# Performance work log

Hardware: AMD Instinct MI355X
Metric: run time of the kernel (lower is better)

The kernel has to match this reference:

```python
import jax, jax.numpy as jnp
import numpy as np

MASK_NEG = 1e30


def setup_inputs() -> dict:
    key = jax.random.key(0)
    k_q, k_k, k_m, k_w1, k_w2, k_v = jax.random.split(key, 6)
    B, S, D, A = 32, 2048, 1024, 1024  # batch, seq, feature dim, attn dim
    # Xavier-uniform-like scale for weights
    lim = float(np.sqrt(6.0 / (D + A)))
    query = jax.random.normal(k_q, (B, D), dtype=jnp.float32)
    keys = jax.random.normal(k_k, (B, S, D), dtype=jnp.float32)
    mask = jax.random.randint(k_m, (B, S), 0, 2) > 0  # True = keep
    W1 = jax.random.uniform(k_w1, (A, D), jnp.float32, -lim, lim)
    W2 = jax.random.uniform(k_w2, (A, D), jnp.float32, -lim, lim)
    v = jax.random.uniform(k_v, (A,), jnp.float32, -lim, lim)
    return {"query": query, "keys": keys, "mask": mask, "W1": W1, "W2": W2, "v": v}


def reference(query, keys, mask, W1, W2, v):
    w1_query = jnp.einsum('bd,ad->ba', query, W1)          # (B, A)
    w2_keys = jnp.einsum('bsd,ad->bsa', keys, W2)          # (B, S, A)
    combined = jnp.tanh(w1_query[:, None, :] + w2_keys)    # (B, S, A)
    scores = jnp.einsum('bsa,a->bs', combined, v)          # (B, S)
    # masked softmax: subtract huge constant at masked-out positions
    scores = scores - (~mask).astype(scores.dtype) * MASK_NEG
    return jax.nn.softmax(scores, axis=-1)
```

## Files before the change

kernel.cpp:

```cpp
#include <hip/hip_runtime.h>
#include <hip/hip_bf16.h>
#include <stdint.h>

#define NB 32
#define NS 2048
#define ND 1024
#define NA 1024
#define MASK_NEG 1e30f

#define BM 256
#define BN 256
#define BK 64
#define NTILES 64

typedef __attribute__((ext_vector_type(4))) float f32x4;
typedef __attribute__((ext_vector_type(8))) __bf16 bf16x8;

__device__ __forceinline__ void glds16(const void* g, void* l) {
  __builtin_amdgcn_global_load_lds(
      (const __attribute__((address_space(1))) uint32_t*)g,
      (__attribute__((address_space(3))) uint32_t*)(uintptr_t)l, 16, 0, 0);
}

__global__ void zero_f32(float* __restrict__ p, int n) {
  int i = blockIdx.x * 256 + threadIdx.x;
  if (i < n) p[i] = 0.f;
}

__global__ __launch_bounds__(256) void cvt_bf16(const float* __restrict__ in,
                                                __bf16* __restrict__ out, int n8) {
  long i = blockIdx.x * 256 + threadIdx.x;
  const long stride = (long)gridDim.x * 256;
  for (; i < n8; i += stride) {
    f32x4 a = ((const f32x4*)in)[2 * i];
    f32x4 b = ((const f32x4*)in)[2 * i + 1];
    bf16x8 o;
#pragma unroll
    for (int j = 0; j < 4; ++j) { o[j] = (__bf16)a[j]; o[4 + j] = (__bf16)b[j]; }
    ((bf16x8*)out)[i] = o;
  }
}

__global__ __launch_bounds__(256) void w1q_kernel(const float* __restrict__ q,
                                                  const float* __restrict__ W1,
                                                  float* __restrict__ w1q) {
  const int b = blockIdx.x;
  const int a0 = blockIdx.y * 64;
  const int t = threadIdx.x;
  const int al = t >> 2;
  const int part = t & 3;
  const float* wrow = W1 + (size_t)(a0 + al) * ND + part * 256;
  const float* qrow = q + (size_t)b * ND + part * 256;
  float sum = 0.f;
#pragma unroll 8
  for (int i = 0; i < 256; i += 4) {
    float4 w = *reinterpret_cast<const float4*>(wrow + i);
    float4 x = *reinterpret_cast<const float4*>(qrow + i);
    sum += w.x * x.x + w.y * x.y + w.z * x.z + w.w * x.w;
  }
  __shared__ float red[256];
  red[t] = sum;
  __syncthreads();
  if (t < 64) {
    w1q[(size_t)b * NA + a0 + t] = red[t * 4] + red[t * 4 + 1] + red[t * 4 + 2] + red[t * 4 + 3];
  }
}

__global__ __launch_bounds__(512, 1) void score_gemm(
    const float* __restrict__ keysf, const __bf16* __restrict__ W2b,
    const float* __restrict__ w1q, const float* __restrict__ vvec,
    float* __restrict__ scores) {
  __shared__ __attribute__((aligned(1024))) char ldsA[6 * 16384];
  __shared__ __attribute__((aligned(1024))) char ldsB[4 * 16384];

  const int t = threadIdx.x;
  const int bs0 = blockIdx.x * BM;
  const int b = bs0 >> 11;
  const int lane = t & 63;
  const int wid = t >> 6;
  const int wr = wid >> 1;
  const int wc = wid & 1;
  const int lrow = lane & 15;
  const int ko = lane >> 4;

  const int rowA = t >> 4;
  const int scolA = (t & 15) ^ (rowA & 15);
  const int rowB = t >> 3;
  const int scolB = (t & 7) ^ (rowB & 7);

  const int sA00 = (ko * 2) ^ lrow, sA01 = (ko * 2 + 1) ^ lrow;
  const int sA10 = (8 + ko * 2) ^ lrow, sA11 = (8 + ko * 2 + 1) ^ lrow;
  const int sB0 = ko ^ (lrow & 7), sB1 = (4 + ko) ^ (lrow & 7);

  f32x4 acc[4][8];
#pragma unroll
  for (int mi = 0; mi < 4; ++mi)
#pragma unroll
    for (int ni = 0; ni < 8; ++ni) acc[mi][ni] = f32x4{0.f, 0.f, 0.f, 0.f};

  bf16x8 af[4][2], bfr[2][2];

#define STAGE_A(T, Q)                                                           \
  do {                                                                          \
    if ((T) < NTILES) {                                                         \
      const unsigned slot_ = (4u * (unsigned)(T) + (unsigned)(Q)) % 6u;         \
      char* d_ = ldsA + slot_ * 16384 + t * 16;                                 \
      const size_t r0_ = (size_t)(bs0 + (Q)*64 + rowA);                         \
      const int kf_ = ((T)&15) * 64 + scolA * 4;                                \
      glds16(keysf + r0_ * ND + kf_, d_);                                       \
      glds16(keysf + (r0_ + 32) * ND + kf_, d_ + 8192);                         \
    }                                                                           \
  } while (0)

#define STAGE_B(T, H)                                                           \
  do {                                                                          \
    if ((T) < NTILES) {                                                         \
      const unsigned slot_ = (2u * (unsigned)(T) + (unsigned)(H)) % 4u;         \
      char* d_ = ldsB + slot_ * 16384 + t * 16;                                 \
      const size_t r0_ = (size_t)(((T) >> 4) * 256 + (H)*128 + rowB);           \
      const int ke_ = (((T)&15) * 64) + scolB * 8;                              \
      glds16(W2b + r0_ * ND + ke_, d_);                                         \
      glds16(W2b + (r0_ + 64) * ND + ke_, d_ + 8192);                           \
    }                                                                           \
  } while (0)

#define SB_ __builtin_amdgcn_sched_barrier(0)
#define P1 __builtin_amdgcn_s_setprio(1)
#define P0 __builtin_amdgcn_s_setprio(0)
#define BAR __builtin_amdgcn_s_barrier()

#define PHASE(P_, STAGES)                                                       \
  do {                                                                          \
    STAGES;                                                                     \
    if ((P_) == 0) {                                                            \
      const char* Ab_ = ldsA + ((4u * (unsigned)tau + (unsigned)wr) % 6u) * 16384; \
      _Pragma("unroll") for (int mi = 0; mi < 4; ++mi) {                        \
        const int rb_ = (mi * 16 + lrow) * 256;                                 \
        f32x4 l0 = *reinterpret_cast<const f32x4*>(Ab_ + rb_ + sA00 * 16);      \
        f32x4 l1 = *reinterpret_cast<const f32x4*>(Ab_ + rb_ + sA01 * 16);      \
        f32x4 h0 = *reinterpret_cast<const f32x4*>(Ab_ + rb_ + sA10 * 16);      \
        f32x4 h1 = *reinterpret_cast<const f32x4*>(Ab_ + rb_ + sA11 * 16);      \
        _Pragma("unroll") for (int j = 0; j < 4; ++j) {                         \
          af[mi][0][j] = (__bf16)l0[j]; af[mi][0][4 + j] = (__bf16)l1[j];       \
          af[mi][1][j] = (__bf16)h0[j]; af[mi][1][4 + j] = (__bf16)h1[j];       \
        }                                                                       \
      }                                                                         \
    }                                                                           \
    {                                                                           \
      const char* Bb_ = ldsB + ((2u * (unsigned)tau + (unsigned)wc) % 4u) * 16384; \
      _Pragma("unroll") for (int nq = 0; nq < 2; ++nq) {                        \
        const int rb_ = (((P_)*2 + nq) * 16 + lrow) * 128;                      \
        bfr[nq][0] = *reinterpret_cast<const bf16x8*>(Bb_ + rb_ + sB0 * 16);    \
        bfr[nq][1] = *reinterpret_cast<const bf16x8*>(Bb_ + rb_ + sB1 * 16);    \
      }                                                                         \
    }                                                                           \
    BAR;                                                                        \
    asm volatile("s_waitcnt lgkmcnt(0)");                                       \
    SB_;                                                                        \
    P1;                                                                         \
    _Pragma("unroll") for (int mi = 0; mi < 4; ++mi)                            \
        _Pragma("unroll") for (int nq = 0; nq < 2; ++nq) {                      \
      acc[mi][(P_)*2 + nq] = __builtin_amdgcn_mfma_f32_16x16x32_bf16(           \
          af[mi][0], bfr[nq][0], acc[mi][(P_)*2 + nq], 0, 0, 0);                \
      acc[mi][(P_)*2 + nq] = __builtin_amdgcn_mfma_f32_16x16x32_bf16(           \
          af[mi][1], bfr[nq][1], acc[mi][(P_)*2 + nq], 0, 0, 0);                \
    }                                                                           \
    P0;                                                                         \
    if ((P_) == 3) {                                                            \
      asm volatile("s_waitcnt vmcnt(0)");                                       \
      SB_;                                                                      \
    }                                                                           \
    BAR;                                                                        \
  } while (0)

  STAGE_A(0, 0);
  STAGE_A(0, 1);
  STAGE_A(0, 2);
  STAGE_A(0, 3);
  STAGE_B(0, 0);
  STAGE_B(0, 1);
  __syncthreads();

  for (int tau = 0; tau < NTILES; ++tau) {
    PHASE(0, { STAGE_A(tau + 1, 0); STAGE_A(tau + 1, 1); STAGE_B(tau + 1, 0); });
    PHASE(1, { STAGE_A(tau + 1, 2); STAGE_A(tau + 1, 3); STAGE_B(tau + 1, 1); });
    PHASE(2, {});
    PHASE(3, {});

    if ((tau & 15) == 15) {
      const int a0 = (tau >> 4) * BN;
      float w1v[8], vv[8];
#pragma unroll
      for (int ni = 0; ni < 8; ++ni) {
        const int a = a0 + wc * 128 + ni * 16 + lrow;
        w1v[ni] = w1q[(size_t)b * NA + a];
        vv[ni] = vvec[a];
      }
#pragma unroll
      for (int mi = 0; mi < 4; ++mi)
#pragma unroll
        for (int r = 0; r < 4; ++r) {
          float p = 0.f;
#pragma unroll
          for (int ni = 0; ni < 8; ++ni) {
            const float x = acc[mi][ni][r] + w1v[ni];
            const float e = __expf(2.f * x);
            p += (1.f - 2.f * __builtin_amdgcn_rcpf(e + 1.f)) * vv[ni];
          }
          p += __shfl_xor(p, 1);
          p += __shfl_xor(p, 2);
          p += __shfl_xor(p, 4);
          p += __shfl_xor(p, 8);
          if (lrow == 0)
            atomicAdd(&scores[bs0 + wr * 64 + mi * 16 + ko * 4 + r], p);
        }
#pragma unroll
      for (int mi = 0; mi < 4; ++mi)
#pragma unroll
        for (int ni = 0; ni < 8; ++ni) acc[mi][ni] = f32x4{0.f, 0.f, 0.f, 0.f};
    }
  }

#undef STAGE_A
#undef STAGE_B
#undef PHASE
#undef SB_
#undef P1
#undef P0
#undef BAR
}

__global__ __launch_bounds__(256) void softmax_kernel(const float* __restrict__ scores,
                                                      const int* __restrict__ mask,
                                                      float* __restrict__ out) {
  const int b = blockIdx.x;
  const int t = threadIdx.x;
  float sc[8];
  float mx = -3.4e38f;
#pragma unroll
  for (int j = 0; j < 8; ++j) {
    int i = t + j * 256;
    float s = scores[b * NS + i];
    if (mask[b * NS + i] == 0) s -= MASK_NEG;
    sc[j] = s;
    mx = fmaxf(mx, s);
  }
#pragma unroll
  for (int off = 1; off < 64; off <<= 1) mx = fmaxf(mx, __shfl_xor(mx, off));
  __shared__ float redm[4];
  __shared__ float reds[4];
  if ((t & 63) == 0) redm[t >> 6] = mx;
  __syncthreads();
  mx = fmaxf(fmaxf(redm[0], redm[1]), fmaxf(redm[2], redm[3]));
  float e[8];
  float sum = 0.f;
#pragma unroll
  for (int j = 0; j < 8; ++j) {
    e[j] = __expf(sc[j] - mx);
    sum += e[j];
  }
#pragma unroll
  for (int off = 1; off < 64; off <<= 1) sum += __shfl_xor(sum, off);
  if ((t & 63) == 0) reds[t >> 6] = sum;
  __syncthreads();
  sum = reds[0] + reds[1] + reds[2] + reds[3];
  float inv = 1.f / sum;
#pragma unroll
  for (int j = 0; j < 8; ++j) out[b * NS + t + j * 256] = e[j] * inv;
}

extern "C" void kernel_launch(void* const* d_in, const int* in_sizes, int n_in,
                              void* d_out, int out_size, void* d_ws, size_t ws_size,
                              hipStream_t stream) {
  const float* q = (const float*)d_in[0];
  const float* keysf = (const float*)d_in[1];
  const int* mask = (const int*)d_in[2];
  const float* W1 = (const float*)d_in[3];
  const float* W2f = (const float*)d_in[4];
  const float* v = (const float*)d_in[5];
  float* out = (float*)d_out;

  float* scores = (float*)d_ws;
  float* w1q = scores + NB * NS;
  __bf16* W2b = (__bf16*)(w1q + NB * NA);

  zero_f32<<<NB * NS / 256, 256, 0, stream>>>(scores, NB * NS);
  cvt_bf16<<<512, 256, 0, stream>>>(W2f, W2b, NA * ND / 8);
  w1q_kernel<<<dim3(NB, NA / 64), 256, 0, stream>>>(q, W1, w1q);
  score_gemm<<<NB * NS / BM, 512, 0, stream>>>(keysf, W2b, w1q, v, scores);
  softmax_kernel<<<NB, 256, 0, stream>>>(scores, mask, out);
}
```

Before: 221.2 us.

## Switch score GEMM from 16x16x32 to 32x32x16 bf16 MFMA tiles

Replaces the 16x16x32 MFMA micro-tiling with 32x32x16 MFMA instructions, reorganising the accumulators into 2x4 f32x16 blocks and reworking the LDS fragment loads and swizzle indexing to match. Each phase now issues 8 larger MFMAs over one k-substep instead of 16 small ones. The epilogue reduction is adapted to the 32-lane row layout, with an extra shuffle and new row indexing for the atomic adds. The aim is to cut the number of B-fragment LDS reads per MFMA and to use the instruction's higher operand reuse, at the cost of different LDS bank access patterns and register pressure.

```diff
diff --git a/kernel.cpp b/kernel.cpp
--- a/kernel.cpp
+++ b/kernel.cpp
@@ -14,6 +14,7 @@
 #define NTILES 64
 
 typedef __attribute__((ext_vector_type(4))) float f32x4;
+typedef __attribute__((ext_vector_type(16))) float f32x16;
 typedef __attribute__((ext_vector_type(8))) __bf16 bf16x8;
 
 __device__ __forceinline__ void glds16(const void* g, void* l) {
@@ -80,25 +81,25 @@
   const int wid = t >> 6;
   const int wr = wid >> 1;
   const int wc = wid & 1;
-  const int lrow = lane & 15;
-  const int ko = lane >> 4;
+  const int r31 = lane & 31;
+  const int hi = lane >> 5;
+  const int lrA = r31 & 15;
+  const int lrB = r31 & 7;
 
   const int rowA = t >> 4;
   const int scolA = (t & 15) ^ (rowA & 15);
   const int rowB = t >> 3;
   const int scolB = (t & 7) ^ (rowB & 7);
 
-  const int sA00 = (ko * 2) ^ lrow, sA01 = (ko * 2 + 1) ^ lrow;
-  const int sA10 = (8 + ko * 2) ^ lrow, sA11 = (8 + ko * 2 + 1) ^ lrow;
-  const int sB0 = ko ^ (lrow & 7), sB1 = (4 + ko) ^ (lrow & 7);
-
-  f32x4 acc[4][8];
-#pragma unroll
-  for (int mi = 0; mi < 4; ++mi)
-#pragma unroll
-    for (int ni = 0; ni < 8; ++ni) acc[mi][ni] = f32x4{0.f, 0.f, 0.f, 0.f};
-
-  bf16x8 af[4][2], bfr[2][2];
+  f32x16 acc[2][4];
+#pragma unroll
+  for (int mi = 0; mi < 2; ++mi)
+#pragma unroll
+    for (int nt = 0; nt < 4; ++nt)
+#pragma unroll
+      for (int r = 0; r < 16; ++r) acc[mi][nt][r] = 0.f;
+
+  bf16x8 af[2][4], bfr[4];
 
 #define STAGE_A(T, Q)                                                           \
   do {                                                                          \
@@ -129,44 +130,42 @@
 #define P0 __builtin_amdgcn_s_setprio(0)
 #define BAR __builtin_amdgcn_s_barrier()
 
-#define PHASE(P_, STAGES)                                                       \
+#define PHASE(KS_, STAGES)                                                      \
   do {                                                                          \
     STAGES;                                                                     \
-    if ((P_) == 0) {                                                            \
+    if ((KS_) == 0) {                                                           \
       const char* Ab_ = ldsA + ((4u * (unsigned)tau + (unsigned)wr) % 6u) * 16384; \
-      _Pragma("unroll") for (int mi = 0; mi < 4; ++mi) {                        \
-        const int rb_ = (mi * 16 + lrow) * 256;                                 \
-        f32x4 l0 = *reinterpret_cast<const f32x4*>(Ab_ + rb_ + sA00 * 16);      \
-        f32x4 l1 = *reinterpret_cast<const f32x4*>(Ab_ + rb_ + sA01 * 16);      \
-        f32x4 h0 = *reinterpret_cast<const f32x4*>(Ab_ + rb_ + sA10 * 16);      \
-        f32x4 h1 = *reinterpret_cast<const f32x4*>(Ab_ + rb_ + sA11 * 16);      \
-        _Pragma("unroll") for (int j = 0; j < 4; ++j) {                         \
-          af[mi][0][j] = (__bf16)l0[j]; af[mi][0][4 + j] = (__bf16)l1[j];       \
-          af[mi][1][j] = (__bf16)h0[j]; af[mi][1][4 + j] = (__bf16)h1[j];       \
+      _Pragma("unroll") for (int mi = 0; mi < 2; ++mi) {                        \
+        const int rb_ = (mi * 32 + r31) * 256;                                  \
+        _Pragma("unroll") for (int ks = 0; ks < 4; ++ks) {                      \
+          const int u0_ = ks * 4 + hi * 2;                                      \
+          f32x4 l0 = *reinterpret_cast<const f32x4*>(Ab_ + rb_ + (u0_ ^ lrA) * 16); \
+          f32x4 l1 = *reinterpret_cast<const f32x4*>(Ab_ + rb_ + ((u0_ + 1) ^ lrA) * 16); \
+          _Pragma("unroll") for (int j = 0; j < 4; ++j) {                       \
+            af[mi][ks][j] = (__bf16)l0[j];                                      \
+            af[mi][ks][4 + j] = (__bf16)l1[j];                                  \
+          }                                                                     \
         }                                                                       \
       }                                                                         \
     }                                                                           \
     {                                                                           \
       const char* Bb_ = ldsB + ((2u * (unsigned)tau + (unsigned)wc) % 4u) * 16384; \
-      _Pragma("unroll") for (int nq = 0; nq < 2; ++nq) {                        \
-        const int rb_ = (((P_)*2 + nq) * 16 + lrow) * 128;                      \
-        bfr[nq][0] = *reinterpret_cast<const bf16x8*>(Bb_ + rb_ + sB0 * 16);    \
-        bfr[nq][1] = *reinterpret_cast<const bf16x8*>(Bb_ + rb_ + sB1 * 16);    \
+      _Pragma("unroll") for (int nt = 0; nt < 4; ++nt) {                        \
+        const int rb_ = (nt * 32 + r31) * 128;                                  \
+        bfr[nt] = *reinterpret_cast<const bf16x8*>(                             \
+            Bb_ + rb_ + (((KS_)*2 + hi) ^ lrB) * 16);                           \
       }                                                                         \
     }                                                                           \
     BAR;                                                                        \
     asm volatile("s_waitcnt lgkmcnt(0)");                                       \
     SB_;                                                                        \
     P1;                                                                         \
-    _Pragma("unroll") for (int mi = 0; mi < 4; ++mi)                            \
-        _Pragma("unroll") for (int nq = 0; nq < 2; ++nq) {                      \
-      acc[mi][(P_)*2 + nq] = __builtin_amdgcn_mfma_f32_16x16x32_bf16(           \
-          af[mi][0], bfr[nq][0], acc[mi][(P_)*2 + nq], 0, 0, 0);                \
-      acc[mi][(P_)*2 + nq] = __builtin_amdgcn_mfma_f32_16x16x32_bf16(           \
-          af[mi][1], bfr[nq][1], acc[mi][(P_)*2 + nq], 0, 0, 0);                \
-    }                                                                           \
+    _Pragma("unroll") for (int mi = 0; mi < 2; ++mi)                            \
+        _Pragma("unroll") for (int nt = 0; nt < 4; ++nt)                        \
+            acc[mi][nt] = __builtin_amdgcn_mfma_f32_32x32x16_bf16(              \
+                af[mi][(KS_)], bfr[nt], acc[mi][nt], 0, 0, 0);                  \
     P0;                                                                         \
-    if ((P_) == 3) {                                                            \
+    if ((KS_) == 3) {                                                           \
       asm volatile("s_waitcnt vmcnt(0)");                                       \
       SB_;                                                                      \
     }                                                                           \
@@ -189,35 +188,37 @@
 
     if ((tau & 15) == 15) {
       const int a0 = (tau >> 4) * BN;
-      float w1v[8], vv[8];
-#pragma unroll
-      for (int ni = 0; ni < 8; ++ni) {
-        const int a = a0 + wc * 128 + ni * 16 + lrow;
-        w1v[ni] = w1q[(size_t)b * NA + a];
-        vv[ni] = vvec[a];
+      float w1v[4], vv[4];
+#pragma unroll
+      for (int nt = 0; nt < 4; ++nt) {
+        const int a = a0 + wc * 128 + nt * 32 + r31;
+        w1v[nt] = w1q[(size_t)b * NA + a];
+        vv[nt] = vvec[a];
       }
 #pragma unroll
-      for (int mi = 0; mi < 4; ++mi)
-#pragma unroll
-        for (int r = 0; r < 4; ++r) {
+      for (int mi = 0; mi < 2; ++mi) {
+#pragma unroll
+        for (int r = 0; r < 16; ++r) {
           float p = 0.f;
 #pragma unroll
-          for (int ni = 0; ni < 8; ++ni) {
-            const float x = acc[mi][ni][r] + w1v[ni];
+          for (int nt = 0; nt < 4; ++nt) {
+            const float x = acc[mi][nt][r] + w1v[nt];
             const float e = __expf(2.f * x);
-            p += (1.f - 2.f * __builtin_amdgcn_rcpf(e + 1.f)) * vv[ni];
+            p += (1.f - 2.f * __builtin_amdgcn_rcpf(e + 1.f)) * vv[nt];
           }
           p += __shfl_xor(p, 1);
           p += __shfl_xor(p, 2);
           p += __shfl_xor(p, 4);
           p += __shfl_xor(p, 8);
-          if (lrow == 0)
-            atomicAdd(&scores[bs0 + wr * 64 + mi * 16 + ko * 4 + r], p);
+          p += __shfl_xor(p, 16);
+          if (r31 == 0)
+            atomicAdd(&scores[bs0 + wr * 64 + mi * 32 + (r & 3) + 8 * (r >> 2) + 4 * hi], p);
         }
 #pragma unroll
-      for (int mi = 0; mi < 4; ++mi)
-#pragma unroll
-        for (int ni = 0; ni < 8; ++ni) acc[mi][ni] = f32x4{0.f, 0.f, 0.f, 0.f};
+        for (int nt = 0; nt < 4; ++nt)
+#pragma unroll
+          for (int r = 0; r < 16; ++r) acc[mi][nt][r] = 0.f;
+      }
     }
   }
 
```

After: 234.3 us. 1.06x slower.
